# Kernel tuning notes

Hardware: AMD Instinct MI355X
Metric: run time of the kernel (lower is better)

Reference implementation:

```python
import jax, jax.numpy as jnp
import numpy as np

UNITS = 64

def _tri_indices(u):
    # pairs (a,b) with b>=a in row-major order == tf.boolean_mask(product_mask1)
    pairs = [(a, b) for a in range(u) for b in range(a, u)]
    ia = np.array([p[0] for p in pairs], np.int32)
    ib = np.array([p[1] for p in pairs], np.int32)
    # triples: for product1 index p=(a,b), keep c>=b (derived from mask2 loops)
    ip, ic = [], []
    for p, (a, b) in enumerate(pairs):
        for c in range(b, u):
            ip.append(p)
            ic.append(c)
    return ia, ib, np.array(ip, np.int32), np.array(ic, np.int32)

def setup_inputs() -> dict:
    key = jax.random.key(0)
    k0, k1, k2, k3, k4 = jax.random.split(key, 5)
    B, D, u = 4096, 66, UNITS
    nprod1 = u * (u + 1) // 2            # 2080
    nprod2 = u * (u + 1) * (u + 2) // 6  # 45760
    inputs = jax.random.normal(k0, (B, D), jnp.float32)
    fw1 = jax.random.uniform(k1, (u,), jnp.float32, 0.0, 2.0 * np.pi * 40.0)
    fw2 = jax.random.normal(k2, (u,), jnp.float32) * 0.05
    fb1 = jax.random.normal(k3, (u,), jnp.float32) * 0.05
    wo = jax.random.normal(k4, (u + nprod1 + nprod2, u), jnp.float32) * 0.05
    return {"inputs": inputs, "fw1": fw1, "fw2": fw2, "fb1": fb1, "wo": wo}

def reference(inputs, fw1, fw2, fb1, wo):
    u = fw1.shape[0]
    ia, ib, ip, ic = _tri_indices(u)
    # Fourier features: cos(x * w1 + b1) * w2,  [B, u]
    f = jnp.cos(inputs[:, :u] * fw1 + fb1) * fw2
    # quadratic upper-triangular products, [B, nprod1] (gather instead of dense outer+mask)
    p1 = f[:, ia] * f[:, ib]
    # cubic products c>=b>=a, [B, nprod2]
    p2 = p1[:, ip] * f[:, ic]
    comb = jnp.concatenate([f, p1, p2], axis=1)  # [B, u+nprod1+nprod2]
    pad = jnp.zeros((inputs.shape[0], inputs.shape[1] - u), inputs.dtype)
    return jnp.concatenate([comb @ wo, pad], axis=1) + inputs
```

## Files before the change

### kernel.cpp

```cpp
#include <hip/hip_runtime.h>
#include <hip/hip_bf16.h>

#define NB      4096
#define ND      66
#define NSTEPP  1792
#define KS      64
#define CH      28
#define MB      32
#define FS      72

#define SBLK    NSTEPP
#define FBLK    (NB*FS/256)
#define PBLK    32

typedef __attribute__((ext_vector_type(8))) _Float16 f16x8;
typedef __attribute__((ext_vector_type(4))) _Float16 f16x4;
typedef __attribute__((ext_vector_type(4))) float    f32x4;

__device__ __attribute__((aligned(16))) _Float16 g_f[NB * FS];
__device__ __attribute__((aligned(16))) _Float16 g_woTi[(size_t)(NSTEPP + 1) * 2048];
__device__ __attribute__((aligned(16))) _Float16 g_part[(size_t)KS * MB * 8192];

__constant__ int c_bb[8] = {0, 48, 204, 532, 1096, 1960, 3188, 4844};

__device__ inline unsigned octet_desc(int o) {
    int t = 0;
#pragma unroll
    for (int i = 1; i < 8; ++i) t += (o >= c_bb[i]);
    int li = o - c_bb[t];
    int P = 8 * t + 8, T = P * (P + 1) / 2;
    int s0, s1;
    if (li == 0)       { s0 = 64; s1 = 64; }
    else if (li <= P)  { s0 = li - 1; s1 = 64; }
    else if (li <= P + T) {
        int r = li - P - 1, a = 0;
        while (r >= P - a) { r -= P - a; ++a; }
        s0 = a; s1 = a + r;
    } else             { s0 = 65; s1 = 65; }
    return (unsigned)s0 | ((unsigned)s1 << 8) | ((unsigned)(8 * t) << 16);
}

__global__ void k_prep(const float* __restrict__ inp, const float* __restrict__ fw1,
                       const float* __restrict__ fw2, const float* __restrict__ fb1,
                       const float* __restrict__ wo, float* __restrict__ out) {
    const int bid = blockIdx.x, tid = threadIdx.x;
    if (bid < SBLK) {
        __shared__ unsigned sd[4];
        if (tid < 4) sd[tid] = octet_desc(bid * 4 + tid);
        __syncthreads();
        const int q = tid >> 6, gg = (tid >> 4) & 3, rl = tid & 15;
        const unsigned d = sd[gg];
        const int s0 = d & 255, s1 = (d >> 8) & 255, cb = d >> 16;
        const int n = q * 16 + rl;
        f16x8 v;
        if (s0 == 64) {
#pragma unroll
            for (int j = 0; j < 8; ++j) v[j] = (_Float16)wo[(cb + j) * 64 + n];
        } else if (s0 < 64 && s1 == 64) {
            int base = 64 + s0 * (129 - s0) / 2 + (cb - s0);
#pragma unroll
            for (int j = 0; j < 8; ++j)
                v[j] = (cb + j >= s0) ? (_Float16)wo[(base + j) * 64 + n] : (_Float16)0.f;
        } else if (s0 < 64) {
            int a = s0, b = s1;
            int TP = 45760 - (64 - a) * (65 - a) * (66 - a) / 6;
            int RB = b * (129 - b) / 2 - a * (129 - a) / 2;
            int base = 2144 + TP + RB + (cb - b);
#pragma unroll
            for (int j = 0; j < 8; ++j)
                v[j] = (cb + j >= b) ? (_Float16)wo[(base + j) * 64 + n] : (_Float16)0.f;
        } else {
#pragma unroll
            for (int j = 0; j < 8; ++j) v[j] = (_Float16)0.f;
        }
        *(f16x8*)(g_woTi + (size_t)bid * 2048 + tid * 8) = v;
    } else if (bid < SBLK + FBLK) {
        int i = (bid - SBLK) * 256 + tid;
        int r = i / FS, c = i - r * FS;
        float v;
        if (c < 64)       v = cosf(inp[r * ND + c] * fw1[c] + fb1[c]) * fw2[c];
        else if (c == 64) v = 1.0f;
        else              v = 0.0f;
        g_f[i] = (_Float16)v;
    } else {
        int i = (bid - SBLK - FBLK) * 256 + tid;
        int r = i >> 1, c = 64 + (i & 1);
        out[r * ND + c] = inp[r * ND + c];
    }
}

__global__ __launch_bounds__(128, 4) void k_gemm() {
    __shared__ __attribute__((aligned(16))) _Float16 fl[128 * FS];
    __shared__ __attribute__((aligned(16))) unsigned ldescT[4 * 32];
    const int mb = blockIdx.x, ks = blockIdx.y, tid = threadIdx.x;
    const int s0c = ks * CH;

    {
        const uint4* src = (const uint4*)(g_f + (size_t)mb * 128 * FS);
        uint4* dst = (uint4*)fl;
        for (int e = tid; e < 128 * FS * 2 / 16; e += 128) dst[e] = src[e];
        {
            int gg = tid >> 5, s = tid & 31;
            ldescT[tid] = (s < CH) ? octet_desc((s0c + s) * 4 + gg) : (65u | (65u << 8));
        }
    }
    __syncthreads();

    const int wave = tid >> 6, lane = tid & 63, rl = lane & 15, g = lane >> 4;
    const _Float16* fr0 = fl + (wave * 64 +  0 + rl) * FS;
    const _Float16* fr1 = fl + (wave * 64 + 16 + rl) * FS;
    const _Float16* fr2 = fl + (wave * 64 + 32 + rl) * FS;
    const _Float16* fr3 = fl + (wave * 64 + 48 + rl) * FS;

    f32x4 acc[4][4];
#pragma unroll
    for (int a = 0; a < 4; ++a)
#pragma unroll
        for (int q = 0; q < 4; ++q) acc[a][q] = f32x4{0.f, 0.f, 0.f, 0.f};

    f16x8 c0{}, c1{}, c2{}, c3{};
    int cbPrev = -1;

#define STEP(dv)                                                               \
    {                                                                          \
        const int si0 = (dv) & 255, si1 = ((dv) >> 8) & 255;                   \
        const int cb = __builtin_amdgcn_readfirstlane((dv) >> 16);             \
        if (cb != cbPrev) {                            \
            cbPrev = cb;                                                       \
            c0 = *(const f16x8*)(fr0 + cb); c1 = *(const f16x8*)(fr1 + cb);    \
            c2 = *(const f16x8*)(fr2 + cb); c3 = *(const f16x8*)(fr3 + cb);    \
        }                                                                      \
        f16x8 nB0 = *(const f16x8*)(bptr +    0);                              \
        f16x8 nB1 = *(const f16x8*)(bptr +  512);                              \
        f16x8 nB2 = *(const f16x8*)(bptr + 1024);                              \
        f16x8 nB3 = *(const f16x8*)(bptr + 1536);                              \
        bptr += 2048;                                                          \
        const _Float16 p0 = fr0[si0] * fr0[si1], p1 = fr1[si0] * fr1[si1];     \
        const _Float16 p2 = fr2[si0] * fr2[si1], p3 = fr3[si0] * fr3[si1];     \
        const f16x8 a0 = c0 * p0, a1 = c1 * p1, a2 = c2 * p2, a3 = c3 * p3;    \
        acc[0][0] = __builtin_amdgcn_mfma_f32_16x16x32_f16(a0, B0, acc[0][0], 0, 0, 0); \
        acc[0][1] = __builtin_amdgcn_mfma_f32_16x16x32_f16(a0, B1, acc[0][1], 0, 0, 0); \
        acc[0][2] = __builtin_amdgcn_mfma_f32_16x16x32_f16(a0, B2, acc[0][2], 0, 0, 0); \
        acc[0][3] = __builtin_amdgcn_mfma_f32_16x16x32_f16(a0, B3, acc[0][3], 0, 0, 0); \
        acc[1][0] = __builtin_amdgcn_mfma_f32_16x16x32_f16(a1, B0, acc[1][0], 0, 0, 0); \
        acc[1][1] = __builtin_amdgcn_mfma_f32_16x16x32_f16(a1, B1, acc[1][1], 0, 0, 0); \
        acc[1][2] = __builtin_amdgcn_mfma_f32_16x16x32_f16(a1, B2, acc[1][2], 0, 0, 0); \
        acc[1][3] = __builtin_amdgcn_mfma_f32_16x16x32_f16(a1, B3, acc[1][3], 0, 0, 0); \
        acc[2][0] = __builtin_amdgcn_mfma_f32_16x16x32_f16(a2, B0, acc[2][0], 0, 0, 0); \
        acc[2][1] = __builtin_amdgcn_mfma_f32_16x16x32_f16(a2, B1, acc[2][1], 0, 0, 0); \
        acc[2][2] = __builtin_amdgcn_mfma_f32_16x16x32_f16(a2, B2, acc[2][2], 0, 0, 0); \
        acc[2][3] = __builtin_amdgcn_mfma_f32_16x16x32_f16(a2, B3, acc[2][3], 0, 0, 0); \
        acc[3][0] = __builtin_amdgcn_mfma_f32_16x16x32_f16(a3, B0, acc[3][0], 0, 0, 0); \
        acc[3][1] = __builtin_amdgcn_mfma_f32_16x16x32_f16(a3, B1, acc[3][1], 0, 0, 0); \
        acc[3][2] = __builtin_amdgcn_mfma_f32_16x16x32_f16(a3, B2, acc[3][2], 0, 0, 0); \
        acc[3][3] = __builtin_amdgcn_mfma_f32_16x16x32_f16(a3, B3, acc[3][3], 0, 0, 0); \
        B0 = nB0; B1 = nB1; B2 = nB2; B3 = nB3;                                \
    }

    const unsigned* dT = ldescT + g * 32;
    const int st = wave * (CH / 2);
#pragma unroll 1
    for (int seg = 0; seg < 2; ++seg) {
        const int sbeg = seg == 0 ? st : 0;
        const int send = seg == 0 ? CH : st;
        if (sbeg >= send) continue;
        const _Float16* bptr = g_woTi + (size_t)(s0c + sbeg) * 2048 + lane * 8;
        f16x8 B0 = *(const f16x8*)(bptr +    0);
        f16x8 B1 = *(const f16x8*)(bptr +  512);
        f16x8 B2 = *(const f16x8*)(bptr + 1024);
        f16x8 B3 = *(const f16x8*)(bptr + 1536);
        bptr += 2048;
#pragma unroll 1
        for (int s2 = sbeg; s2 < send; s2 += 2) {
            uint2 dd = *(const uint2*)(dT + s2);
            STEP(dd.x);
            STEP(dd.y);
        }
    }
#undef STEP

    _Float16* pp = g_part + ((size_t)ks * MB + mb) * 8192 + wave * 4096;
#pragma unroll
    for (int a = 0; a < 4; ++a)
#pragma unroll
        for (int q = 0; q < 4; ++q) {
            f16x4 v;
            v[0] = (_Float16)acc[a][q][0]; v[1] = (_Float16)acc[a][q][1];
            v[2] = (_Float16)acc[a][q][2]; v[3] = (_Float16)acc[a][q][3];
            *(f16x4*)(pp + (a * 4 + q) * 256 + lane * 4) = v;
        }
}

__global__ void k_reduce(const float* __restrict__ inp, float* __restrict__ out) {
    int t = blockIdx.x * 256 + threadIdx.x;
    int c = t & 63, rg = t >> 6;
    int mb = rg >> 5, wave = (rg >> 4) & 1, a = (rg >> 2) & 3, g = rg & 3;
    int q = c >> 4, rl = c & 15, lane = g * 16 + rl;
    int rbase = mb * 128 + wave * 64 + a * 16 + g * 4;
    float acc[4];
#pragma unroll
    for (int i2 = 0; i2 < 4; ++i2) acc[i2] = inp[(rbase + i2) * ND + c];
    const _Float16* pp = g_part + (size_t)mb * 8192 + wave * 4096
                       + (a * 4 + q) * 256 + lane * 4;
#pragma unroll
    for (int ks = 0; ks < KS; ++ks) {
        const f16x4 p = *(const f16x4*)(pp + (size_t)ks * MB * 8192);
#pragma unroll
        for (int i2 = 0; i2 < 4; ++i2) acc[i2] += (float)p[i2];
    }
#pragma unroll
    for (int i2 = 0; i2 < 4; ++i2) out[(rbase + i2) * ND + c] = acc[i2];
}

extern "C" void kernel_launch(void* const* d_in, const int* in_sizes, int n_in,
                              void* d_out, int out_size, void* d_ws, size_t ws_size,
                              hipStream_t stream) {
    const float* inp = (const float*)d_in[0];
    const float* fw1 = (const float*)d_in[1];
    const float* fw2 = (const float*)d_in[2];
    const float* fb1 = (const float*)d_in[3];
    const float* wo  = (const float*)d_in[4];
    float* out = (float*)d_out;

    k_prep<<<SBLK + FBLK + PBLK, 256, 0, stream>>>(inp, fw1, fw2, fb1, wo, out);
    k_gemm<<<dim3(MB, KS), 128, 0, stream>>>();
    k_reduce<<<256, 256, 0, stream>>>(inp, out);
}
```

Measured before the change: 50.62 us.

## Triple-buffer weight loads in GEMM loop and drop staggered wave start

Replaces the one-step-ahead prefetch of B fragments with a three-deep rotating register buffer, so each weight step's global load is issued three steps before its MFMAs. Both waves now walk the 28 steps in the same order instead of starting at staggered offsets. The launch bound is lowered to 3 blocks per SM to give room for the extra registers, and the weight buffer is padded so the over-fetch past the last step stays in bounds. The trade-off is lower occupancy and losing the cache-spreading effect of the staggered start.

```diff
diff --git a/kernel.cpp b/kernel.cpp
--- a/kernel.cpp
+++ b/kernel.cpp
@@ -18,7 +18,7 @@
 typedef __attribute__((ext_vector_type(4))) float    f32x4;
 
 __device__ __attribute__((aligned(16))) _Float16 g_f[NB * FS];
-__device__ __attribute__((aligned(16))) _Float16 g_woTi[(size_t)(NSTEPP + 1) * 2048];
+__device__ __attribute__((aligned(16))) _Float16 g_woTi[(size_t)(NSTEPP + 8) * 2048];
 __device__ __attribute__((aligned(16))) _Float16 g_part[(size_t)KS * MB * 8192];
 
 __constant__ int c_bb[8] = {0, 48, 204, 532, 1096, 1960, 3188, 4844};
@@ -89,7 +89,7 @@
     }
 }
 
-__global__ __launch_bounds__(128, 4) void k_gemm() {
+__global__ __launch_bounds__(128, 3) void k_gemm() {
     __shared__ __attribute__((aligned(16))) _Float16 fl[128 * FS];
     __shared__ __attribute__((aligned(16))) unsigned ldescT[4 * 32];
     const int mb = blockIdx.x, ks = blockIdx.y, tid = threadIdx.x;
@@ -120,64 +120,64 @@
 
     f16x8 c0{}, c1{}, c2{}, c3{};
     int cbPrev = -1;
-
-#define STEP(dv)                                                               \
+    const unsigned* dT = ldescT + g * 32;
+    const _Float16* wob = g_woTi + (size_t)s0c * 2048 + lane * 8;
+
+#define LOADB(Q0, Q1, Q2, Q3, sidx)                                            \
     {                                                                          \
-        const int si0 = (dv) & 255, si1 = ((dv) >> 8) & 255;                   \
-        const int cb = __builtin_amdgcn_readfirstlane((dv) >> 16);             \
+        const _Float16* bp = wob + (size_t)(sidx) * 2048;                      \
+        Q0 = *(const f16x8*)(bp +    0);                                       \
+        Q1 = *(const f16x8*)(bp +  512);                                       \
+        Q2 = *(const f16x8*)(bp + 1024);                                       \
+        Q3 = *(const f16x8*)(bp + 1536);                                       \
+    }
+
+#define COMP(sidx, Q0, Q1, Q2, Q3)                                             \
+    {                                                                          \
+        const unsigned dv = dT[sidx];                                          \
+        const int si0 = dv & 255, si1 = (dv >> 8) & 255;                       \
+        const int cb = __builtin_amdgcn_readfirstlane(dv >> 16);               \
         if (cb != cbPrev) {                            \
             cbPrev = cb;                                                       \
             c0 = *(const f16x8*)(fr0 + cb); c1 = *(const f16x8*)(fr1 + cb);    \
             c2 = *(const f16x8*)(fr2 + cb); c3 = *(const f16x8*)(fr3 + cb);    \
         }                                                                      \
-        f16x8 nB0 = *(const f16x8*)(bptr +    0);                              \
-        f16x8 nB1 = *(const f16x8*)(bptr +  512);                              \
-        f16x8 nB2 = *(const f16x8*)(bptr + 1024);                              \
-        f16x8 nB3 = *(const f16x8*)(bptr + 1536);                              \
-        bptr += 2048;                                                          \
         const _Float16 p0 = fr0[si0] * fr0[si1], p1 = fr1[si0] * fr1[si1];     \
         const _Float16 p2 = fr2[si0] * fr2[si1], p3 = fr3[si0] * fr3[si1];     \
         const f16x8 a0 = c0 * p0, a1 = c1 * p1, a2 = c2 * p2, a3 = c3 * p3;    \
-        acc[0][0] = __builtin_amdgcn_mfma_f32_16x16x32_f16(a0, B0, acc[0][0], 0, 0, 0); \
-        acc[0][1] = __builtin_amdgcn_mfma_f32_16x16x32_f16(a0, B1, acc[0][1], 0, 0, 0); \
-        acc[0][2] = __builtin_amdgcn_mfma_f32_16x16x32_f16(a0, B2, acc[0][2], 0, 0, 0); \
-        acc[0][3] = __builtin_amdgcn_mfma_f32_16x16x32_f16(a0, B3, acc[0][3], 0, 0, 0); \
-        acc[1][0] = __builtin_amdgcn_mfma_f32_16x16x32_f16(a1, B0, acc[1][0], 0, 0, 0); \
-        acc[1][1] = __builtin_amdgcn_mfma_f32_16x16x32_f16(a1, B1, acc[1][1], 0, 0, 0); \
-        acc[1][2] = __builtin_amdgcn_mfma_f32_16x16x32_f16(a1, B2, acc[1][2], 0, 0, 0); \
-        acc[1][3] = __builtin_amdgcn_mfma_f32_16x16x32_f16(a1, B3, acc[1][3], 0, 0, 0); \
-        acc[2][0] = __builtin_amdgcn_mfma_f32_16x16x32_f16(a2, B0, acc[2][0], 0, 0, 0); \
-        acc[2][1] = __builtin_amdgcn_mfma_f32_16x16x32_f16(a2, B1, acc[2][1], 0, 0, 0); \
-        acc[2][2] = __builtin_amdgcn_mfma_f32_16x16x32_f16(a2, B2, acc[2][2], 0, 0, 0); \
-        acc[2][3] = __builtin_amdgcn_mfma_f32_16x16x32_f16(a2, B3, acc[2][3], 0, 0, 0); \
-        acc[3][0] = __builtin_amdgcn_mfma_f32_16x16x32_f16(a3, B0, acc[3][0], 0, 0, 0); \
-        acc[3][1] = __builtin_amdgcn_mfma_f32_16x16x32_f16(a3, B1, acc[3][1], 0, 0, 0); \
-        acc[3][2] = __builtin_amdgcn_mfma_f32_16x16x32_f16(a3, B2, acc[3][2], 0, 0, 0); \
-        acc[3][3] = __builtin_amdgcn_mfma_f32_16x16x32_f16(a3, B3, acc[3][3], 0, 0, 0); \
-        B0 = nB0; B1 = nB1; B2 = nB2; B3 = nB3;                                \
-    }
-
-    const unsigned* dT = ldescT + g * 32;
-    const int st = wave * (CH / 2);
+        acc[0][0] = __builtin_amdgcn_mfma_f32_16x16x32_f16(a0, Q0, acc[0][0], 0, 0, 0); \
+        acc[0][1] = __builtin_amdgcn_mfma_f32_16x16x32_f16(a0, Q1, acc[0][1], 0, 0, 0); \
+        acc[0][2] = __builtin_amdgcn_mfma_f32_16x16x32_f16(a0, Q2, acc[0][2], 0, 0, 0); \
+        acc[0][3] = __builtin_amdgcn_mfma_f32_16x16x32_f16(a0, Q3, acc[0][3], 0, 0, 0); \
+        acc[1][0] = __builtin_amdgcn_mfma_f32_16x16x32_f16(a1, Q0, acc[1][0], 0, 0, 0); \
+        acc[1][1] = __builtin_amdgcn_mfma_f32_16x16x32_f16(a1, Q1, acc[1][1], 0, 0, 0); \
+        acc[1][2] = __builtin_amdgcn_mfma_f32_16x16x32_f16(a1, Q2, acc[1][2], 0, 0, 0); \
+        acc[1][3] = __builtin_amdgcn_mfma_f32_16x16x32_f16(a1, Q3, acc[1][3], 0, 0, 0); \
+        acc[2][0] = __builtin_amdgcn_mfma_f32_16x16x32_f16(a2, Q0, acc[2][0], 0, 0, 0); \
+        acc[2][1] = __builtin_amdgcn_mfma_f32_16x16x32_f16(a2, Q1, acc[2][1], 0, 0, 0); \
+        acc[2][2] = __builtin_amdgcn_mfma_f32_16x16x32_f16(a2, Q2, acc[2][2], 0, 0, 0); \
+        acc[2][3] = __builtin_amdgcn_mfma_f32_16x16x32_f16(a2, Q3, acc[2][3], 0, 0, 0); \
+        acc[3][0] = __builtin_amdgcn_mfma_f32_16x16x32_f16(a3, Q0, acc[3][0], 0, 0, 0); \
+        acc[3][1] = __builtin_amdgcn_mfma_f32_16x16x32_f16(a3, Q1, acc[3][1], 0, 0, 0); \
+        acc[3][2] = __builtin_amdgcn_mfma_f32_16x16x32_f16(a3, Q2, acc[3][2], 0, 0, 0); \
+        acc[3][3] = __builtin_amdgcn_mfma_f32_16x16x32_f16(a3, Q3, acc[3][3], 0, 0, 0); \
+    }
+
+    f16x8 x0, x1, x2, x3, y0, y1, y2, y3, z0, z1, z2, z3;
+    LOADB(x0, x1, x2, x3, 0)
+    LOADB(y0, y1, y2, y3, 1)
+    LOADB(z0, z1, z2, z3, 2)
+    int s = 0;
 #pragma unroll 1
-    for (int seg = 0; seg < 2; ++seg) {
-        const int sbeg = seg == 0 ? st : 0;
-        const int send = seg == 0 ? CH : st;
-        if (sbeg >= send) continue;
-        const _Float16* bptr = g_woTi + (size_t)(s0c + sbeg) * 2048 + lane * 8;
-        f16x8 B0 = *(const f16x8*)(bptr +    0);
-        f16x8 B1 = *(const f16x8*)(bptr +  512);
-        f16x8 B2 = *(const f16x8*)(bptr + 1024);
-        f16x8 B3 = *(const f16x8*)(bptr + 1536);
-        bptr += 2048;
-#pragma unroll 1
-        for (int s2 = sbeg; s2 < send; s2 += 2) {
-            uint2 dd = *(const uint2*)(dT + s2);
-            STEP(dd.x);
-            STEP(dd.y);
-        }
-    }
-#undef STEP
+    for (int i = 0; i < 9; ++i) {
+        COMP(s,     x0, x1, x2, x3) LOADB(x0, x1, x2, x3, s + 3)
+        COMP(s + 1, y0, y1, y2, y3) LOADB(y0, y1, y2, y3, s + 4)
+        COMP(s + 2, z0, z1, z2, z3) LOADB(z0, z1, z2, z3, s + 5)
+        s += 3;
+    }
+    COMP(27, x0, x1, x2, x3)
+#undef LOADB
+#undef COMP
 
     _Float16* pp = g_part + ((size_t)ks * MB + mb) * 8192 + wave * 4096;
 #pragma unroll
```

New measurement: 51.40 us. Within noise of the previous version (+1.5%).
